# Kernel tuning notes

Hardware: AMD Instinct MI355X
Metric: run time of the kernel (lower is better)

The kernel has to match this reference:

```python
import jax, jax.numpy as jnp
import numpy as np

B, L, C, H, W = 2, 32, 128, 32, 32
R_MIN, R_MAX = 0.8, 0.99


def setup_inputs() -> dict:
    key = jax.random.key(0)
    ks = jax.random.split(key, 12)
    x = jax.random.normal(ks[0], (B, L, C, H, W), jnp.float32)
    # LRU initialization exactly as in the torch module
    u1 = jax.random.uniform(ks[1], (C, H), jnp.float32)
    u2 = jax.random.uniform(ks[2], (C, H), jnp.float32)
    nu_log = jnp.log(-0.5 * jnp.log(u1 * (R_MAX**2 - R_MIN**2) + R_MIN**2))
    theta_log = jnp.log(u2 * 2.0 * jnp.pi)
    abs_lam = jnp.exp(-jnp.exp(nu_log))  # |lambda| = exp(-nu)
    gamma_log = jnp.log(jnp.sqrt(1.0 - abs_lam**2))
    params_log = jnp.concatenate([nu_log, theta_log, gamma_log], axis=0)  # [3C, H]
    s = 0.05
    Wb_re = jax.random.normal(ks[3], (C, C), jnp.float32) * s
    Wb_im = jax.random.normal(ks[4], (C, C), jnp.float32) * s
    bb_re = jax.random.normal(ks[5], (C,), jnp.float32) * s
    bb_im = jax.random.normal(ks[6], (C,), jnp.float32) * s
    Wc_re = jax.random.normal(ks[7], (C, C), jnp.float32) * s
    Wc_im = jax.random.normal(ks[8], (C, C), jnp.float32) * s
    bc_re = jax.random.normal(ks[9], (C,), jnp.float32) * s
    bc_im = jax.random.normal(ks[10], (C,), jnp.float32) * s
    ln_w = jnp.ones((C, H, W), jnp.float32)
    ln_b = jnp.zeros((C, H, W), jnp.float32)
    return dict(x=x, params_log=params_log, Wb_re=Wb_re, Wb_im=Wb_im, bb_re=bb_re,
                bb_im=bb_im, Wc_re=Wc_re, Wc_im=Wc_im, bc_re=bc_re, bc_im=bc_im,
                ln_w=ln_w, ln_b=ln_b)


def reference(x, params_log, Wb_re, Wb_im, bb_re, bb_im, Wc_re, Wc_im, bc_re, bc_im, ln_w, ln_b):
    Cn = x.shape[2]
    nu = jnp.exp(params_log[:Cn])           # [C,H]
    theta = jnpp_exp = jnp.exp(params_log[Cn:2 * Cn])
    gamma = jnp.exp(params_log[2 * Cn:])    # [C,H]
    lam = jnp.exp(-nu + 1j * theta)         # [C,H] complex, |lam|<1

    # FFT2 over spatial dims
    h = jnp.fft.fft2(x.astype(jnp.complex64))  # [B,L,C,H,W]
    # complex 1x1 conv proj_B (CxC GEMM per pixel)
    Wb = (Wb_re + 1j * Wb_im).astype(jnp.complex64)
    bb = (bb_re + 1j * bb_im).astype(jnp.complex64)
    h = jnp.einsum('oc,blchw->blohw', Wb, h) + bb[None, None, :, None, None]
    # gamma gating, broadcast over B,L,W
    h = h * gamma[None, None, :, :, None]

    # linear recurrence y_t = lam * y_{t-1} + h_t (pscan), lam constant in t
    lam_b = lam[None, :, :, None]  # [1,C,H,1] broadcasts over [B,C,H,W]
    def step(carry, ht):
        y = lam_b * carry + ht
        return y, y
    h_t = jnp.moveaxis(h, 1, 0)  # [L,B,C,H,W]
    _, ys = jax.lax.scan(step, jnp.zeros_like(h_t[0]), h_t)
    h = jnp.moveaxis(ys, 0, 1)   # [B,L,C,H,W]
    last_hidden_out = h[:, -1:]

    h = jnp.fft.ifft2(h)
    Wc = (Wc_re + 1j * Wc_im).astype(jnp.complex64)
    bc = (bc_re + 1j * bc_im).astype(jnp.complex64)
    h = jnp.einsum('oc,blchw->blohw', Wc, h) + bc[None, None, :, None, None]
    h = h.real  # real cast, dropout is identity in eval

    # LayerNorm over (C,H,W) jointly
    mean = jnp.mean(h, axis=(2, 3, 4), keepdims=True)
    var = jnp.var(h, axis=(2, 3, 4), keepdims=True)
    h = (h - mean) / jnp.sqrt(var + 1e-5) * ln_w + ln_b
    return h + x, last_hidden_out
```

## Files before the change

### kernel.cpp

```cpp
#include <hip/hip_runtime.h>
#include <cstdint>
#include <cstddef>

#define DEVINL __device__ __forceinline__

static constexpr int Bdim = 2, Ldim = 32, Cdim = 128, Hdim = 32, Wdim = 32;
static constexpr int HW  = Hdim * Wdim;
static constexpr int CHW = Cdim * HW;
static constexpr size_t OUT0_ELEMS = (size_t)Bdim * Ldim * CHW;
static constexpr size_t OUT1_CPLX  = (size_t)Bdim * CHW;

typedef __attribute__((ext_vector_type(8))) short short8v;
typedef __attribute__((ext_vector_type(4))) float f32x4;

DEVINL int bitrev5(int v) {
    return ((v&1)<<4) | ((v&2)<<2) | (v&4) | ((v&8)>>2) | ((v&16)>>4);
}
DEVINL unsigned short f2bf(float v) {
    unsigned u = __float_as_uint(v);
    return (unsigned short)((u + 0x7FFFu + ((u >> 16) & 1u)) >> 16);
}
DEVINL float bf2f(unsigned short b) { return __uint_as_float(((unsigned)b) << 16); }
DEVINL void bfsplit(float v, short& hi, short& lo) {
    unsigned short hb = f2bf(v);
    hi = (short)hb;
    float hf = bf2f(hb);
    lo = (short)f2bf(v - hf);
}
DEVINL unsigned pack2bf(float2 v) {
    return (unsigned)f2bf(v.x) | ((unsigned)f2bf(v.y) << 16);
}
DEVINL float2 unpack2bf(unsigned u) {
    return make_float2(__uint_as_float(u << 16), __uint_as_float(u & 0xFFFF0000u));
}

template<int INV>
DEVINL void fft32_reg(float2 v[32]) {
    constexpr float TC[16] = { 1.0f, 0.980785280f, 0.923879533f, 0.831469612f,
                               0.707106781f, 0.555570233f, 0.382683432f, 0.195090322f,
                               0.0f, -0.195090322f, -0.382683432f, -0.555570233f,
                              -0.707106781f, -0.831469612f, -0.923879533f, -0.980785280f };
    constexpr float TS[16] = { 0.0f, -0.195090322f, -0.382683432f, -0.555570233f,
                              -0.707106781f, -0.831469612f, -0.923879533f, -0.980785280f,
                              -1.0f, -0.980785280f, -0.923879533f, -0.831469612f,
                              -0.707106781f, -0.555570233f, -0.382683432f, -0.195090322f };
#pragma unroll
    for (int st = 0; st < 5; ++st) {
        const int half = 1 << st;
#pragma unroll
        for (int bf = 0; bf < 16; ++bf) {
            const int g = bf >> st;
            const int j = bf & (half - 1);
            const int i0 = (g << (st+1)) + j;
            const float wr = TC[j << (4-st)];
            const float wi = INV ? -TS[j << (4-st)] : TS[j << (4-st)];
            float2 a0 = v[i0], a1 = v[i0+half];
            float tr = wr*a1.x - wi*a1.y;
            float ti = wr*a1.y + wi*a1.x;
            v[i0]      = make_float2(a0.x+tr, a0.y+ti);
            v[i0+half] = make_float2(a0.x-tr, a0.y-ti);
        }
    }
}


__global__ __launch_bounds__(256) void fft_pack_fwd_kernel(const float* __restrict__ x,
                                                           short* __restrict__ P) {
    __shared__ short T[32][2][2][16][8];
    const int blk = blockIdx.x;
    const int bl = blk >> 4, cg = blk & 15;
    const int t = threadIdx.x;
    const int ci = t >> 5, w = t & 31;
    const int c = cg*8 + ci;
    const float* src = x + ((size_t)(bl*Cdim + c))*HW + w;
    float2 v[32];
#pragma unroll
    for (int i = 0; i < 32; ++i)
        v[i] = make_float2(src[(size_t)bitrev5(i)*Wdim], 0.f);
    fft32_reg<0>(v);
#pragma unroll
    for (int h = 0; h < 32; ++h) {
        T[h][0][w>>4][w&15][ci] = (short)f2bf(v[h].x);
        T[h][1][w>>4][w&15][ci] = (short)f2bf(v[h].y);
    }
    __syncthreads();
    const int kc0 = cg >> 2, lnb = (cg & 3) * 16;
#pragma unroll
    for (int p = 0; p < 8; ++p) {
        const int lin = p*256 + t;
        const int h = lin >> 6, rem = lin & 63;
        const int pl = rem >> 5, nt = (rem >> 4) & 1, wl = rem & 15;
        const float4 val = *reinterpret_cast<const float4*>(&T[h][pl][nt][wl][0]);
        const size_t dst = ((size_t)(bl*32 + h)*8 + kc0 + pl*4)*1024
                         + (size_t)nt*512 + (size_t)(lnb + wl)*8;
        *reinterpret_cast<float4*>(P + dst) = val;
    }
}

__global__ __launch_bounds__(256) void ifft_pack_kernel(const unsigned* __restrict__ Hf2,
                                                        short* __restrict__ P) {
    __shared__ short T[32][2][2][16][8];
    const int blk = blockIdx.x;
    const int bl = blk >> 4, cg = blk & 15;
    const int t = threadIdx.x;
    const int ci = t >> 5, w = t & 31;
    const int c = cg*8 + ci;
    const unsigned* src = Hf2 + ((size_t)(bl*Cdim + c))*HW + w;
    float2 v[32];
#pragma unroll
    for (int i = 0; i < 32; ++i) v[i] = unpack2bf(src[(size_t)bitrev5(i)*Wdim]);
    fft32_reg<1>(v);
    const float sc = 1.0f / 32.0f;
#pragma unroll
    for (int h = 0; h < 32; ++h) {
        T[h][0][w>>4][w&15][ci] = (short)f2bf(v[h].x * sc);
        T[h][1][w>>4][w&15][ci] = (short)f2bf(v[h].y * sc);
    }
    __syncthreads();
    const int kc0 = cg >> 2, lnb = (cg & 3) * 16;
#pragma unroll
    for (int p = 0; p < 8; ++p) {
        const int lin = p*256 + t;
        const int h = lin >> 6, rem = lin & 63;
        const int pl = rem >> 5, nt = (rem >> 4) & 1, wl = rem & 15;
        const float4 val = *reinterpret_cast<const float4*>(&T[h][pl][nt][wl][0]);
        const size_t dst = ((size_t)(bl*32 + h)*8 + kc0 + pl*4)*1024
                         + (size_t)nt*512 + (size_t)(lnb + wl)*8;
        *reinterpret_cast<float4*>(P + dst) = val;
    }
}

template<int CPLX>
__global__ __launch_bounds__(256) void fft_w_out1_kernel(const float2* __restrict__ st31,
                                                         float* __restrict__ out1) {
    const int row = blockIdx.x*256 + threadIdx.x;
    const float2* src = st31 + (size_t)row*32;
    float2 v[32];
#pragma unroll
    for (int i = 0; i < 32; ++i) v[i] = src[bitrev5(i)];
    fft32_reg<0>(v);
    if (CPLX) {
        float2* dst = reinterpret_cast<float2*>(out1) + (size_t)row*32;
#pragma unroll
        for (int i = 0; i < 32; ++i) dst[i] = v[i];
    } else {
        float* dst = out1 + (size_t)row*32;
#pragma unroll
        for (int i = 0; i < 32; ++i) dst[i] = v[i].x;
    }
}

__global__ __launch_bounds__(256) void pack_w_kernel(
    const float* __restrict__ Wb_re, const float* __restrict__ Wb_im,
    const float* __restrict__ Wc_re, const float* __restrict__ Wc_im,
    short* __restrict__ Apack)
{
    const int gid = blockIdx.x*256 + threadIdx.x;
    const int a    = gid >> 12;
    const int rem  = gid & 4095;
    const int f    = rem >> 6;
    const int lane = rem & 63;
    const int m  = f >> 3, kc = f & 7;
    const int row = m*16 + (lane & 15);
    const int kbase = kc*32 + ((lane >> 4) << 3);
    short8v hi8, lo8;
#pragma unroll
    for (int j = 0; j < 8; ++j) {
        const int k = kbase + j;
        const int half = k >> 7;
        const int c = k & 127;
        float v;
        if (a == 0)      v = half ? -Wb_im[row*Cdim + c] : Wb_re[row*Cdim + c];
        else if (a == 1) v = half ?  Wb_re[row*Cdim + c] : Wb_im[row*Cdim + c];
        else             v = half ? -Wc_im[row*Cdim + c] : Wc_re[row*Cdim + c];
        short h, l; bfsplit(v, h, l);
        hi8[j] = h; lo8[j] = l;
    }
    const size_t off = (size_t)(f*64 + lane)*8;
    *reinterpret_cast<short8v*>(Apack + (size_t)(2*a)  *32768 + off) = hi8;
    *reinterpret_cast<short8v*>(Apack + (size_t)(2*a+1)*32768 + off) = lo8;
}

template<int MODE>
__global__ __launch_bounds__(256) void mix_mfma2_kernel(
    const short* __restrict__ Pin,
    unsigned* __restrict__ Hf2,
    const short* __restrict__ Apack,
    const float* __restrict__ bre, const float* __restrict__ bim,
    const float* __restrict__ pl,
    unsigned short* __restrict__ outr,
    float2* __restrict__ lnpart)
{
    __shared__ short Bs[8][4][64][8];
    const int bx = blockIdx.x;
    const int bl = bx >> 4, tt = bx & 15;
    const int t = threadIdx.x;
    const int wv = t >> 6, lane = t & 63;

    const short* src = Pin + (size_t)(bl*32 + tt*2)*8192;
#pragma unroll
    for (int q = 0; q < 8; ++q) {
        const int u = q*256 + t;
        const int kc = u >> 8, nt4 = (u >> 6) & 3, ln = u & 63;
        const short* s = src + (size_t)(nt4 >> 1)*8192 + kc*1024 + (nt4 & 1)*512 + ln*8;
        *reinterpret_cast<float4*>(&Bs[kc][nt4][ln][0]) =
            *reinterpret_cast<const float4*>(s);
    }
    __syncthreads();

    f32x4 accRe[2][4];
    f32x4 accIm[2][4];
#pragma unroll
    for (int mi = 0; mi < 2; ++mi)
#pragma unroll
        for (int nt = 0; nt < 4; ++nt) {
            accRe[mi][nt] = (f32x4)(0.0f);
            accIm[mi][nt] = (f32x4)(0.0f);
        }

    const short* Are_hi = Apack + (MODE == 0 ? 0 : 4)*32768;
    const short* Are_lo = Are_hi + 32768;
    const short* Aim_hi = Apack + 2*32768;
    const short* Aim_lo = Aim_hi + 32768;

#pragma unroll 2
    for (int kc = 0; kc < 8; ++kc) {
        short8v bh[4];
#pragma unroll
        for (int nt = 0; nt < 4; ++nt)
            bh[nt] = *reinterpret_cast<const short8v*>(&Bs[kc][nt][lane][0]);
#pragma unroll
        for (int mi = 0; mi < 2; ++mi) {
            const int m = wv*2 + mi;
            const size_t off = (size_t)((m*8 + kc)*64 + lane)*8;
            const short8v arh = *reinterpret_cast<const short8v*>(Are_hi + off);
            const short8v arl = *reinterpret_cast<const short8v*>(Are_lo + off);
#pragma unroll
            for (int nt = 0; nt < 4; ++nt) {
                accRe[mi][nt] = __builtin_amdgcn_mfma_f32_16x16x32_bf16(arh, bh[nt], accRe[mi][nt], 0, 0, 0);
                accRe[mi][nt] = __builtin_amdgcn_mfma_f32_16x16x32_bf16(arl, bh[nt], accRe[mi][nt], 0, 0, 0);
            }
            if (MODE == 0) {
                const short8v aih = *reinterpret_cast<const short8v*>(Aim_hi + off);
                const short8v ail = *reinterpret_cast<const short8v*>(Aim_lo + off);
#pragma unroll
                for (int nt = 0; nt < 4; ++nt) {
                    accIm[mi][nt] = __builtin_amdgcn_mfma_f32_16x16x32_bf16(aih, bh[nt], accIm[mi][nt], 0, 0, 0);
                    accIm[mi][nt] = __builtin_amdgcn_mfma_f32_16x16x32_bf16(ail, bh[nt], accIm[mi][nt], 0, 0, 0);
                }
            }
        }
    }

    const int col   = lane & 15;
    const int rbase = (lane >> 4) * 4;
    float lns = 0.f, lnq = 0.f;
#pragma unroll
    for (int mi = 0; mi < 2; ++mi) {
#pragma unroll
        for (int r = 0; r < 4; ++r) {
            const int o = wv*32 + mi*16 + rbase + r;
            if (MODE == 0) {
                const float br = bre[o], bi = bim[o];
                const float g0 = expf(pl[(2*Cdim + o)*Hdim + 2*tt]);
                const float g1 = expf(pl[(2*Cdim + o)*Hdim + 2*tt + 1]);
#pragma unroll
                for (int nt = 0; nt < 4; ++nt) {
                    const int wcol = nt*16 + col;
                    const float g = (nt < 2) ? g0 : g1;
                    const float bsel = ((wcol & 31) == 0) ? 1.0f : 0.0f;
                    float2 rv;
                    rv.x = (accRe[mi][nt][r] + br*bsel) * g;
                    rv.y = (accIm[mi][nt][r] + bi*bsel) * g;
                    Hf2[(size_t)bl*CHW + (size_t)o*HW + tt*64 + wcol] = pack2bf(rv);
                }
            } else {
                const float br = bre[o];
#pragma unroll
                for (int nt = 0; nt < 4; ++nt) {
                    const int wcol = nt*16 + col;
                    const float v = accRe[mi][nt][r] + br;
                    outr[(size_t)bl*CHW + (size_t)o*HW + tt*64 + wcol] = f2bf(v);
                    lns += v; lnq += v*v;
                }
            }
        }
    }
    if (MODE == 1) {
#pragma unroll
        for (int off = 32; off > 0; off >>= 1) {
            lns += __shfl_down(lns, off);
            lnq += __shfl_down(lnq, off);
        }
        __shared__ float2 red[4];
        if (lane == 0) red[wv] = make_float2(lns, lnq);
        __syncthreads();
        if (t == 0) {
            float2 a = red[0], b2 = red[1], c2 = red[2], d = red[3];
            lnpart[bx] = make_float2(a.x + b2.x + c2.x + d.x, a.y + b2.y + c2.y + d.y);
        }
    }
}

__global__ __launch_bounds__(256) void scan_kernel(
    unsigned* __restrict__ Hf2, const float* __restrict__ pl, float2* __restrict__ st31)
{
    const int idx = blockIdx.x*256 + threadIdx.x;
    const int b   = idx >> 17;
    const int chw = idx & (CHW - 1);
    const int c   = chw >> 10;
    const int h   = (chw >> 5) & 31;
    const float nu = expf(pl[c*Hdim + h]);
    const float th = expf(pl[(Cdim + c)*Hdim + h]);
    const float rr = expf(-nu);
    const float lr = rr * cosf(th);
    const float li = rr * sinf(th);
    float2 y = make_float2(0.f, 0.f);
    const size_t basei = (size_t)b * Ldim * CHW + chw;
#pragma unroll 4
    for (int l = 0; l < Ldim; ++l) {
        float2 hv = unpack2bf(Hf2[basei + (size_t)l*CHW]);
        float yr = fmaf(lr, y.x, fmaf(-li, y.y, hv.x));
        float yi = fmaf(lr, y.y, fmaf( li, y.x, hv.y));
        y = make_float2(yr, yi);
        Hf2[basei + (size_t)l*CHW] = pack2bf(y);
    }
    st31[(size_t)b*CHW + chw] = y;
}

__global__ __launch_bounds__(64) void ln_finish_kernel(const float2* __restrict__ lnpart,
                                                       float2* __restrict__ stats) {
    const int bl = blockIdx.x;
    const int t = threadIdx.x;
    float s = 0.f, sq = 0.f;
    if (t < 16) { float2 v = lnpart[bl*16 + t]; s = v.x; sq = v.y; }
#pragma unroll
    for (int off = 8; off > 0; off >>= 1) {
        s  += __shfl_down(s, off);
        sq += __shfl_down(sq, off);
    }
    if (t == 0) {
        const float invN = 1.0f / (float)CHW;
        float mean = s * invN;
        float var  = sq * invN - mean*mean;
        stats[bl] = make_float2(mean, rsqrtf(var + 1e-5f));
    }
}

__global__ __launch_bounds__(256) void ln_apply_kernel(
    float* __restrict__ out0, const unsigned short* __restrict__ hpre,
    const float* __restrict__ x,
    const float* __restrict__ lnw, const float* __restrict__ lnb,
    const float2* __restrict__ stats)
{
    const int idx4 = blockIdx.x*256 + threadIdx.x;
    const int i = idx4 * 4;
    const int bl = i >> 17;
    const int chw4 = (i & (CHW - 1)) >> 2;
    const float2 st = stats[bl];
    const uint2 hu = reinterpret_cast<const uint2*>(hpre)[idx4];
    float4 h;
    h.x = __uint_as_float(hu.x << 16);
    h.y = __uint_as_float(hu.x & 0xFFFF0000u);
    h.z = __uint_as_float(hu.y << 16);
    h.w = __uint_as_float(hu.y & 0xFFFF0000u);
    float4 xv = reinterpret_cast<const float4*>(x)[idx4];
    float4 w  = reinterpret_cast<const float4*>(lnw)[chw4];
    float4 bb = reinterpret_cast<const float4*>(lnb)[chw4];
    const float m = st.x, rs = st.y;
    float4 r;
    r.x = fmaf((h.x - m)*rs, w.x, bb.x) + xv.x;
    r.y = fmaf((h.y - m)*rs, w.y, bb.y) + xv.y;
    r.z = fmaf((h.z - m)*rs, w.z, bb.z) + xv.z;
    r.w = fmaf((h.w - m)*rs, w.w, bb.w) + xv.w;
    reinterpret_cast<float4*>(out0)[idx4] = r;
}

extern "C" void kernel_launch(void* const* d_in, const int* in_sizes, int n_in,
                              void* d_out, int out_size, void* d_ws, size_t ws_size,
                              hipStream_t stream)
{
    const float* x     = (const float*)d_in[0];
    const float* pl    = (const float*)d_in[1];
    const float* Wb_re = (const float*)d_in[2];
    const float* Wb_im = (const float*)d_in[3];
    const float* bb_re = (const float*)d_in[4];
    const float* bb_im = (const float*)d_in[5];
    const float* Wc_re = (const float*)d_in[6];
    const float* Wc_im = (const float*)d_in[7];
    const float* bc_re = (const float*)d_in[8];
    const float* bc_im = (const float*)d_in[9];
    const float* ln_w  = (const float*)d_in[10];
    const float* ln_b  = (const float*)d_in[11];

    float* out0 = (float*)d_out;
    float* out1 = out0 + OUT0_ELEMS;

    char* ws = (char*)d_ws;
    short*          P       = (short*)          ws;
    unsigned*       Hf2     = (unsigned*)       (ws + 33554432);
    unsigned short* out0pre = (unsigned short*) (ws + 67108864);
    float2*         st31    = (float2*)         (ws + 83886080);
    short*          Apack   = (short*)          (ws + 85983232);
    float2*         lnpart  = (float2*)         (ws + 86376448);
    float2*         stats   = (float2*)         (ws + 86384640);

    const bool interleaved = ((size_t)out_size >= OUT0_ELEMS + 2*OUT1_CPLX);

    pack_w_kernel<<<48, 256, 0, stream>>>(Wb_re, Wb_im, Wc_re, Wc_im, Apack);
    fft_pack_fwd_kernel<<<1024, 256, 0, stream>>>(x, P);
    mix_mfma2_kernel<0><<<1024, 256, 0, stream>>>(P, Hf2, Apack, bb_re, bb_im, pl, nullptr, nullptr);
    scan_kernel<<<1024, 256, 0, stream>>>(Hf2, pl, st31);
    if (interleaved)
        fft_w_out1_kernel<1><<<32, 256, 0, stream>>>(st31, out1);
    else
        fft_w_out1_kernel<0><<<32, 256, 0, stream>>>(st31, out1);
    ifft_pack_kernel<<<1024, 256, 0, stream>>>(Hf2, P);
    mix_mfma2_kernel<1><<<1024, 256, 0, stream>>>(P, nullptr, Apack, bc_re, bc_im, pl, out0pre, lnpart);
    ln_finish_kernel<<<64, 64, 0, stream>>>(lnpart, stats);
    ln_apply_kernel<<<8192, 256, 0, stream>>>(out0, out0pre, x, ln_w, ln_b, stats);
}
```

Measured before the change: 108.7 us.

## Fuse scan with inverse H-FFT and gather packed bf16 in mix kernel

```diff
diff --git a/kernel.cpp b/kernel.cpp
--- a/kernel.cpp
+++ b/kernel.cpp
@@ -20,11 +20,10 @@
     unsigned u = __float_as_uint(v);
     return (unsigned short)((u + 0x7FFFu + ((u >> 16) & 1u)) >> 16);
 }
-DEVINL float bf2f(unsigned short b) { return __uint_as_float(((unsigned)b) << 16); }
 DEVINL void bfsplit(float v, short& hi, short& lo) {
     unsigned short hb = f2bf(v);
     hi = (short)hb;
-    float hf = bf2f(hb);
+    float hf = __uint_as_float(((unsigned)hb) << 16);
     lo = (short)f2bf(v - hf);
 }
 DEVINL unsigned pack2bf(float2 v) {
@@ -63,71 +62,20 @@
     }
 }
 
-
-__global__ __launch_bounds__(256) void fft_pack_fwd_kernel(const float* __restrict__ x,
-                                                           short* __restrict__ P) {
-    __shared__ short T[32][2][2][16][8];
-    const int blk = blockIdx.x;
-    const int bl = blk >> 4, cg = blk & 15;
-    const int t = threadIdx.x;
-    const int ci = t >> 5, w = t & 31;
-    const int c = cg*8 + ci;
-    const float* src = x + ((size_t)(bl*Cdim + c))*HW + w;
+__global__ __launch_bounds__(256) void fft_h_fwd_bf_kernel(const float* __restrict__ x,
+                                                           unsigned* __restrict__ Hf) {
+    const int gid = blockIdx.x*256 + threadIdx.x;
+    const int w = gid & 31;
+    const size_t slice = (size_t)(gid >> 5);
+    const float* src = x + slice*HW + w;
     float2 v[32];
 #pragma unroll
     for (int i = 0; i < 32; ++i)
         v[i] = make_float2(src[(size_t)bitrev5(i)*Wdim], 0.f);
     fft32_reg<0>(v);
-#pragma unroll
-    for (int h = 0; h < 32; ++h) {
-        T[h][0][w>>4][w&15][ci] = (short)f2bf(v[h].x);
-        T[h][1][w>>4][w&15][ci] = (short)f2bf(v[h].y);
-    }
-    __syncthreads();
-    const int kc0 = cg >> 2, lnb = (cg & 3) * 16;
-#pragma unroll
-    for (int p = 0; p < 8; ++p) {
-        const int lin = p*256 + t;
-        const int h = lin >> 6, rem = lin & 63;
-        const int pl = rem >> 5, nt = (rem >> 4) & 1, wl = rem & 15;
-        const float4 val = *reinterpret_cast<const float4*>(&T[h][pl][nt][wl][0]);
-        const size_t dst = ((size_t)(bl*32 + h)*8 + kc0 + pl*4)*1024
-                         + (size_t)nt*512 + (size_t)(lnb + wl)*8;
-        *reinterpret_cast<float4*>(P + dst) = val;
-    }
-}
-
-__global__ __launch_bounds__(256) void ifft_pack_kernel(const unsigned* __restrict__ Hf2,
-                                                        short* __restrict__ P) {
-    __shared__ short T[32][2][2][16][8];
-    const int blk = blockIdx.x;
-    const int bl = blk >> 4, cg = blk & 15;
-    const int t = threadIdx.x;
-    const int ci = t >> 5, w = t & 31;
-    const int c = cg*8 + ci;
-    const unsigned* src = Hf2 + ((size_t)(bl*Cdim + c))*HW + w;
-    float2 v[32];
-#pragma unroll
-    for (int i = 0; i < 32; ++i) v[i] = unpack2bf(src[(size_t)bitrev5(i)*Wdim]);
-    fft32_reg<1>(v);
-    const float sc = 1.0f / 32.0f;
-#pragma unroll
-    for (int h = 0; h < 32; ++h) {
-        T[h][0][w>>4][w&15][ci] = (short)f2bf(v[h].x * sc);
-        T[h][1][w>>4][w&15][ci] = (short)f2bf(v[h].y * sc);
-    }
-    __syncthreads();
-    const int kc0 = cg >> 2, lnb = (cg & 3) * 16;
-#pragma unroll
-    for (int p = 0; p < 8; ++p) {
-        const int lin = p*256 + t;
-        const int h = lin >> 6, rem = lin & 63;
-        const int pl = rem >> 5, nt = (rem >> 4) & 1, wl = rem & 15;
-        const float4 val = *reinterpret_cast<const float4*>(&T[h][pl][nt][wl][0]);
-        const size_t dst = ((size_t)(bl*32 + h)*8 + kc0 + pl*4)*1024
-                         + (size_t)nt*512 + (size_t)(lnb + wl)*8;
-        *reinterpret_cast<float4*>(P + dst) = val;
-    }
+    unsigned* dst = Hf + slice*HW + w;
+#pragma unroll
+    for (int h = 0; h < 32; ++h) dst[(size_t)h*Wdim] = pack2bf(v[h]);
 }
 
 template<int CPLX>
@@ -182,9 +130,9 @@
 }
 
 template<int MODE>
-__global__ __launch_bounds__(256) void mix_mfma2_kernel(
-    const short* __restrict__ Pin,
-    unsigned* __restrict__ Hf2,
+__global__ __launch_bounds__(256) void mix_mfma3_kernel(
+    const unsigned* __restrict__ Yin,
+    unsigned* __restrict__ Sout,
     const short* __restrict__ Apack,
     const float* __restrict__ bre, const float* __restrict__ bim,
     const float* __restrict__ pl,
@@ -197,14 +145,27 @@
     const int t = threadIdx.x;
     const int wv = t >> 6, lane = t & 63;
 
-    const short* src = Pin + (size_t)(bl*32 + tt*2)*8192;
-#pragma unroll
-    for (int q = 0; q < 8; ++q) {
-        const int u = q*256 + t;
-        const int kc = u >> 8, nt4 = (u >> 6) & 3, ln = u & 63;
-        const short* s = src + (size_t)(nt4 >> 1)*8192 + kc*1024 + (nt4 & 1)*512 + ln*8;
-        *reinterpret_cast<float4*>(&Bs[kc][nt4][ln][0]) =
-            *reinterpret_cast<const float4*>(s);
+    const unsigned* src = Yin + (size_t)bl*CHW + tt*64;
+#pragma unroll
+    for (int g = 0; g < 4; ++g) {
+        const int id = g*256 + t;
+        const int hw = id & 63;
+        const int co = id >> 6;
+        const int kc = co >> 2;
+        const int ln = (co & 3)*16 + (hw & 15);
+        const int nt4 = hw >> 4;
+        unsigned u[8];
+#pragma unroll
+        for (int j = 0; j < 8; ++j)
+            u[j] = src[(size_t)(co*8 + j)*HW + hw];
+        unsigned re[4], im[4];
+#pragma unroll
+        for (int p = 0; p < 4; ++p) {
+            re[p] = (u[2*p] & 0xFFFFu) | (u[2*p+1] << 16);
+            im[p] = (u[2*p] >> 16) | (u[2*p+1] & 0xFFFF0000u);
+        }
+        *reinterpret_cast<uint4*>(&Bs[kc][nt4][ln][0])   = make_uint4(re[0], re[1], re[2], re[3]);
+        *reinterpret_cast<uint4*>(&Bs[kc+4][nt4][ln][0]) = make_uint4(im[0], im[1], im[2], im[3]);
     }
     __syncthreads();
 
@@ -272,7 +233,7 @@
                     float2 rv;
                     rv.x = (accRe[mi][nt][r] + br*bsel) * g;
                     rv.y = (accIm[mi][nt][r] + bi*bsel) * g;
-                    Hf2[(size_t)bl*CHW + (size_t)o*HW + tt*64 + wcol] = pack2bf(rv);
+                    Sout[(size_t)bl*CHW + (size_t)o*HW + tt*64 + wcol] = pack2bf(rv);
                 }
             } else {
                 const float br = bre[o];
@@ -302,30 +263,78 @@
     }
 }
 
-__global__ __launch_bounds__(256) void scan_kernel(
-    unsigned* __restrict__ Hf2, const float* __restrict__ pl, float2* __restrict__ st31)
+__global__ __launch_bounds__(256) void scan_ifft_kernel(
+    const unsigned* __restrict__ Sin,
+    unsigned* __restrict__ Ysp,
+    const float* __restrict__ pl,
+    float2* __restrict__ st31)
 {
-    const int idx = blockIdx.x*256 + threadIdx.x;
-    const int b   = idx >> 17;
-    const int chw = idx & (CHW - 1);
-    const int c   = chw >> 10;
-    const int h   = (chw >> 5) & 31;
-    const float nu = expf(pl[c*Hdim + h]);
-    const float th = expf(pl[(Cdim + c)*Hdim + h]);
-    const float rr = expf(-nu);
-    const float lr = rr * cosf(th);
-    const float li = rr * sinf(th);
-    float2 y = make_float2(0.f, 0.f);
-    const size_t basei = (size_t)b * Ldim * CHW + chw;
-#pragma unroll 4
+    __shared__ float2 sh[32][33];
+    __shared__ float2 tw[16];
+    const int blk = blockIdx.x;
+    const int b = blk >> 7, c = blk & 127;
+    const int t = threadIdx.x;
+    const int s = t >> 5, w = t & 31;
+    if (t < 16) {
+        float a = -6.283185307179586f * (float)t / 32.0f;
+        tw[t] = make_float2(cosf(a), sinf(a));
+    }
+    int hb[4]; float2 lam[4]; float2 y[4];
+#pragma unroll
+    for (int j = 0; j < 4; ++j) {
+        hb[j] = bitrev5(4*s + j);
+        const float nu = expf(pl[c*Hdim + hb[j]]);
+        const float th = expf(pl[(Cdim + c)*Hdim + hb[j]]);
+        const float r = expf(-nu);
+        lam[j] = make_float2(r*cosf(th), r*sinf(th));
+        y[j] = make_float2(0.f, 0.f);
+    }
+    const float sc = 1.0f / 32.0f;
     for (int l = 0; l < Ldim; ++l) {
-        float2 hv = unpack2bf(Hf2[basei + (size_t)l*CHW]);
-        float yr = fmaf(lr, y.x, fmaf(-li, y.y, hv.x));
-        float yi = fmaf(lr, y.y, fmaf( li, y.x, hv.y));
-        y = make_float2(yr, yi);
-        Hf2[basei + (size_t)l*CHW] = pack2bf(y);
-    }
-    st31[(size_t)b*CHW + chw] = y;
+        const size_t base = ((size_t)(b*Ldim + l)*Cdim + c)*HW;
+#pragma unroll
+        for (int j = 0; j < 4; ++j) {
+            float2 hv = unpack2bf(Sin[base + (size_t)hb[j]*Wdim + w]);
+            float yr = fmaf(lam[j].x, y[j].x, fmaf(-lam[j].y, y[j].y, hv.x));
+            float yi = fmaf(lam[j].x, y[j].y, fmaf( lam[j].y, y[j].x, hv.y));
+            y[j] = make_float2(yr, yi);
+            sh[4*s + j][w] = y[j];
+        }
+        __syncthreads();
+#pragma unroll
+        for (int st = 0; st < 5; ++st) {
+            const int half = 1 << st;
+#pragma unroll
+            for (int q = 0; q < 2; ++q) {
+                int bid = t + q*256;
+                int col = bid & 31;
+                int bf  = bid >> 5;
+                int g = bf >> st;
+                int jj = bf & (half - 1);
+                int i0 = (g << (st+1)) + jj;
+                float2 tww = tw[jj << (4-st)];
+                tww.y = -tww.y;
+                float2 a0 = sh[i0][col];
+                float2 a1 = sh[i0 + half][col];
+                float tr = tww.x*a1.x - tww.y*a1.y;
+                float ti = tww.x*a1.y + tww.y*a1.x;
+                sh[i0][col]        = make_float2(a0.x + tr, a0.y + ti);
+                sh[i0 + half][col] = make_float2(a0.x - tr, a0.y - ti);
+            }
+            __syncthreads();
+        }
+#pragma unroll
+        for (int j = 0; j < 4; ++j) {
+            float2 v = sh[4*s + j][w];
+            Ysp[base + (size_t)(4*s + j)*Wdim + w] =
+                pack2bf(make_float2(v.x*sc, v.y*sc));
+        }
+        __syncthreads();
+    }
+    const size_t obase = ((size_t)b*Cdim + c)*HW;
+#pragma unroll
+    for (int j = 0; j < 4; ++j)
+        st31[obase + (size_t)hb[j]*Wdim + w] = y[j];
 }
 
 __global__ __launch_bounds__(64) void ln_finish_kernel(const float2* __restrict__ lnpart,
@@ -397,8 +406,8 @@
     float* out1 = out0 + OUT0_ELEMS;
 
     char* ws = (char*)d_ws;
-    short*          P       = (short*)          ws;
-    unsigned*       Hf2     = (unsigned*)       (ws + 33554432);
+    unsigned*       bufA    = (unsigned*)       ws;
+    unsigned*       bufB    = (unsigned*)       (ws + 33554432);
     unsigned short* out0pre = (unsigned short*) (ws + 67108864);
     float2*         st31    = (float2*)         (ws + 83886080);
     short*          Apack   = (short*)          (ws + 85983232);
@@ -408,15 +417,14 @@
     const bool interleaved = ((size_t)out_size >= OUT0_ELEMS + 2*OUT1_CPLX);
 
     pack_w_kernel<<<48, 256, 0, stream>>>(Wb_re, Wb_im, Wc_re, Wc_im, Apack);
-    fft_pack_fwd_kernel<<<1024, 256, 0, stream>>>(x, P);
-    mix_mfma2_kernel<0><<<1024, 256, 0, stream>>>(P, Hf2, Apack, bb_re, bb_im, pl, nullptr, nullptr);
-    scan_kernel<<<1024, 256, 0, stream>>>(Hf2, pl, st31);
+    fft_h_fwd_bf_kernel<<<1024, 256, 0, stream>>>(x, bufA);
+    mix_mfma3_kernel<0><<<1024, 256, 0, stream>>>(bufA, bufB, Apack, bb_re, bb_im, pl, nullptr, nullptr);
+    scan_ifft_kernel<<<256, 256, 0, stream>>>(bufB, bufA, pl, st31);
     if (interleaved)
         fft_w_out1_kernel<1><<<32, 256, 0, stream>>>(st31, out1);
     else
         fft_w_out1_kernel<0><<<32, 256, 0, stream>>>(st31, out1);
-    ifft_pack_kernel<<<1024, 256, 0, stream>>>(Hf2, P);
-    mix_mfma2_kernel<1><<<1024, 256, 0, stream>>>(P, nullptr, Apack, bc_re, bc_im, pl, out0pre, lnpart);
+    mix_mfma3_kernel<1><<<1024, 256, 0, stream>>>(bufA, nullptr, Apack, bc_re, bc_im, pl, out0pre, lnpart);
     ln_finish_kernel<<<64, 64, 0, stream>>>(lnpart, stats);
     ln_apply_kernel<<<8192, 256, 0, stream>>>(out0, out0pre, x, ln_w, ln_b, stats);
 }
```

After: 135.4 us. 1.25x slower.
